# Performance work log

Hardware: AMD Instinct MI355X
Metric: run time of the kernel (lower is better)

The kernel has to match this reference:

```python
import jax, jax.numpy as jnp
import numpy as np

N_NODES, N_EDGES, N_GRAPHS = 5000, 80000, 64
LATENT, HID, STEPS = 128, 512, 3


def _mlp(h, Ws, bs):
    # MLP: ReLU after every linear (incl. last) -- MLPwoLastAct is the variant without it
    for W, b in zip(Ws, bs):
        h = jax.nn.relu(h @ W + b)
    return h


def _mlp_wo_last_act(h, Ws, bs):
    n = len(Ws)
    for i, (W, b) in enumerate(zip(Ws, bs)):
        h = h @ W + b
        if i < n - 1:
            h = jax.nn.relu(h)
    return h


def setup_inputs() -> dict:
    key = jax.random.key(0)
    ks = iter(jax.random.split(key, 64))

    def nrm(shape, s=0.05):
        return (jax.random.normal(next(ks), shape) * s).astype(jnp.float32)

    inp = {}
    inp["x"] = jax.random.normal(next(ks), (N_NODES, LATENT), jnp.float32)
    inp["edge_index"] = jax.random.randint(next(ks), (2, N_EDGES), 0, N_NODES, jnp.int32)
    inp["edge_attr"] = jax.random.normal(next(ks), (N_EDGES, LATENT), jnp.float32)
    inp["u"] = jax.random.normal(next(ks), (N_GRAPHS, LATENT), jnp.float32)
    inp["node_batch"] = jnp.sort(jax.random.randint(next(ks), (N_NODES,), 0, N_GRAPHS, jnp.int32))
    inp["edge_batch"] = jnp.sort(jax.random.randint(next(ks), (N_EDGES,), 0, N_GRAPHS, jnp.int32))
    inp["pos"] = jax.random.normal(next(ks), (N_NODES, 3), jnp.float32)
    inp["last_pos_init"] = jax.random.uniform(next(ks), (N_NODES, 3), jnp.float32, -1.0, 1.0)

    # PosEmbeddingwithMask: pos MLP(3->128->128), dis MLP(1->128->128)
    inp["pos_emb_W1"], inp["pos_emb_b1"] = nrm((3, LATENT)), nrm((LATENT,))
    inp["pos_emb_W2"], inp["pos_emb_b2"] = nrm((LATENT, LATENT)), nrm((LATENT,))
    inp["dis_W1"], inp["dis_b1"] = nrm((1, LATENT)), nrm((LATENT,))
    inp["dis_W2"], inp["dis_b2"] = nrm((LATENT, LATENT)), nrm((LATENT,))

    # per-layer edge / node MLPs: (4*latent) -> 512 -> 512 -> 128, stacked over STEPS
    cin = 4 * LATENT
    for pre in ("edge", "node"):
        inp[f"{pre}_W1"], inp[f"{pre}_b1"] = nrm((STEPS, cin, HID)), nrm((STEPS, HID))
        inp[f"{pre}_W2"], inp[f"{pre}_b2"] = nrm((STEPS, HID, HID)), nrm((STEPS, HID))
        inp[f"{pre}_W3"], inp[f"{pre}_b3"] = nrm((STEPS, HID, LATENT)), nrm((STEPS, LATENT))

    # global MLP only for layers 0..STEPS-2: (3*latent) -> 512 -> 512 -> 128
    gL, gin = STEPS - 1, 3 * LATENT
    inp["glob_W1"], inp["glob_b1"] = nrm((gL, gin, HID)), nrm((gL, HID))
    inp["glob_W2"], inp["glob_b2"] = nrm((gL, HID, HID)), nrm((gL, HID))
    inp["glob_W3"], inp["glob_b3"] = nrm((gL, HID, LATENT)), nrm((gL, LATENT))

    # shared pos_decoder: MLPwoLastAct(128 -> 128 -> 3)
    inp["dec_W1"], inp["dec_b1"] = nrm((LATENT, LATENT)), nrm((LATENT,))
    inp["dec_W2"], inp["dec_b2"] = nrm((LATENT, 3)), nrm((3,))
    return inp


def reference(x, edge_index, edge_attr, u, node_batch, edge_batch, pos, last_pos_init,
              pos_emb_W1, pos_emb_b1, pos_emb_W2, pos_emb_b2,
              dis_W1, dis_b1, dis_W2, dis_b2,
              edge_W1, edge_b1, edge_W2, edge_b2, edge_W3, edge_b3,
              node_W1, node_b1, node_W2, node_b2, node_W3, node_b3,
              glob_W1, glob_b1, glob_W2, glob_b2, glob_W3, glob_b3,
              dec_W1, dec_b1, dec_W2, dec_b2):
    src, dst = edge_index[0], edge_index[1]
    N = x.shape[0]
    counts = jnp.maximum(
        jax.ops.segment_sum(jnp.ones((N, 1), x.dtype), node_batch, N_GRAPHS), 1.0)

    def move2origin(p):
        mean = jax.ops.segment_sum(p, node_batch, N_GRAPHS) / counts
        return p - mean[node_batch]

    xs, es, us = x, edge_attr, u
    last_pos = last_pos_init  # pos_new_zeros.uniform_(-1, 1), materialized as input
    pos_preds = []
    for l in range(STEPS):
        p = last_pos  # mode='mol2conf': pos = last_pred
        # PosEmbeddingwithMask
        ex = xs + _mlp(p, (pos_emb_W1, pos_emb_W2), (pos_emb_b1, pos_emb_b2))
        length = jnp.linalg.norm(p[src] - p[dst], axis=-1, keepdims=True)  # [E,1]
        ee = es + _mlp(length, (dis_W1, dis_W2), (dis_b1, dis_b2))
        # edge update: gather -> MLP
        edge_in = jnp.concatenate([ex[src], ex[dst], ee, us[edge_batch]], axis=-1)
        e1 = _mlp(edge_in, (edge_W1[l], edge_W2[l], edge_W3[l]),
                  (edge_b1[l], edge_b2[l], edge_b3[l]))
        # scatter-reduce (sum) to nodes, then node MLP
        sent = jax.ops.segment_sum(e1, src, N)
        recv = jax.ops.segment_sum(e1, dst, N)
        node_in = jnp.concatenate([ex, sent, recv, us[node_batch]], axis=-1)
        x1 = _mlp(node_in, (node_W1[l], node_W2[l], node_W3[l]),
                  (node_b1[l], node_b2[l], node_b3[l]))
        # global update (None on last layer)
        if l < STEPS - 1:
            g_in = jnp.concatenate([us,
                                    jax.ops.segment_sum(x1, node_batch, N_GRAPHS),
                                    jax.ops.segment_sum(e1, edge_batch, N_GRAPHS)], axis=-1)
            u1 = _mlp(g_in, (glob_W1[l], glob_W2[l], glob_W3[l]),
                      (glob_b1[l], glob_b2[l], glob_b3[l]))
        else:
            u1 = us
        # residuals (dropout is identity in eval)
        xs, es, us = x1 + xs, e1 + es, u1 + us
        # pred_pos_residual=True
        delta = _mlp_wo_last_act(xs, (dec_W1, dec_W2), (dec_b1, dec_b2))
        last_pos = move2origin(last_pos + delta)
        pos_preds.append(last_pos)
    return xs, es, us, jnp.stack(pos_preds)
```

## Files before the change

### kernel.cpp

```cpp
#include <hip/hip_runtime.h>
#include <hip/hip_bf16.h>
#include <stdint.h>

#define NN 5000
#define NE 80000
#define NG 64
#define LAT 128
#define HIDN 512

typedef __hip_bfloat16 bf16;
typedef short short8 __attribute__((ext_vector_type(8)));
typedef float f32x4 __attribute__((ext_vector_type(4)));

__device__ __forceinline__ float b2f(bf16 v) { return __bfloat162float(v); }
__device__ __forceinline__ bf16 f2b(float v) { return __float2bfloat16(v); }
__device__ __forceinline__ short f2bs(float v) {
    bf16 b = __float2bfloat16(v);
    short s; __builtin_memcpy(&s, &b, 2); return s;
}

template<int K, int MODE>
__global__ __launch_bounds__(256)
void gemm_kernel(const bf16* __restrict__ A,
                 const bf16* __restrict__ Bt,
                 const float* __restrict__ bias,
                 const float* residf, const bf16* residb,
                 float* out_sf, bf16* out_sb, bf16* out_rb,
                 int M, int N, int nnt,
                 const int* __restrict__ g_src, const int* __restrict__ g_dst,
                 const int* __restrict__ g_eb,
                 const bf16* __restrict__ g_ex, const bf16* __restrict__ g_ee,
                 const bf16* __restrict__ g_us,
                 const float* __restrict__ lp,
                 const float* __restrict__ aW, const float* __restrict__ ab)
{
    constexpr bool HASA = (MODE <= 1);
    __shared__ __align__(16) bf16 As[HASA ? 128 * 32 : 8];
    __shared__ __align__(16) bf16 Bs[128 * 32];
    const int tid  = threadIdx.x;
    const int lane = tid & 63;
    const int w    = tid >> 6;
    const int li   = lane & 15, grp = lane >> 4;
    const int wr   = w >> 1, wc = w & 1;

    const int nb  = gridDim.x;
    const int q   = nb >> 3, r = nb & 7;
    const int xcd = blockIdx.x & 7, jj = blockIdx.x >> 3;
    const int wg  = (xcd < r ? xcd * (q + 1) : r * (q + 1) + (xcd - r) * q) + jj;
    const int m0  = (wg / nnt) * 128;
    const int n0  = (wg % nnt) * 128;

    f32x4 acc[4][4];
#pragma unroll
    for (int m = 0; m < 4; ++m)
#pragma unroll
        for (int n = 0; n < 4; ++n)
            acc[m][n] = (f32x4){0.f, 0.f, 0.f, 0.f};

    float r0[4], r1[4], r2[4];
    if (MODE == 2) {
#pragma unroll
        for (int m = 0; m < 4; ++m) {
            int rr = m0 + wr * 64 + m * 16 + li; if (rr >= M) rr = M - 1;
            r0[m] = lp[rr * 3 + 0]; r1[m] = lp[rr * 3 + 1]; r2[m] = lp[rr * 3 + 2];
        }
    } else if (MODE == 3) {
#pragma unroll
        for (int m = 0; m < 4; ++m) {
            int rr = m0 + wr * 64 + m * 16 + li; if (rr >= M) rr = M - 1;
            const int s = g_src[rr], d = g_dst[rr];
            const float dx = lp[s*3+0] - lp[d*3+0];
            const float dy = lp[s*3+1] - lp[d*3+1];
            const float dz = lp[s*3+2] - lp[d*3+2];
            r0[m] = sqrtf(dx*dx + dy*dy + dz*dz);
        }
    }

    const int offBase = w * 1024 + lane * 16;

    for (int kt = 0; kt < K / 32; ++kt) {
        if (HASA) {
#pragma unroll
            for (int c = 0; c < 2; ++c) {
                const int off = offBase + c * 4096;
                const int rr_ = off >> 6;
                const int g   = (off >> 4) & 3;
                const int gl  = g ^ ((rr_ >> 1) & 3);
                const int klocal = gl * 8;
                const bf16* srcp;
                if (MODE == 1) {
                    int e = m0 + rr_; if (e >= M) e = M - 1;
                    const int seg = kt >> 2;
                    const int so  = ((kt & 3) << 5) + klocal;
                    if (seg == 0)      srcp = g_ex + (size_t)g_src[e] * LAT + so;
                    else if (seg == 1) srcp = g_ex + (size_t)g_dst[e] * LAT + so;
                    else if (seg == 2) srcp = g_ee + (size_t)e * LAT + so;
                    else               srcp = g_us + (size_t)g_eb[e] * LAT + so;
                } else {
                    int rr = m0 + rr_; if (rr >= M) rr = M - 1;
                    srcp = A + (size_t)rr * K + kt * 32 + klocal;
                }
                __builtin_amdgcn_global_load_lds(
                    (__attribute__((address_space(1))) const void*)srcp,
                    (__attribute__((address_space(3))) void*)((char*)As + off),
                    16, 0, 0);
            }
        }
#pragma unroll
        for (int c = 0; c < 2; ++c) {
            const int off = offBase + c * 4096;
            const int rr_ = off >> 6;
            const int g   = (off >> 4) & 3;
            const int gl  = g ^ ((rr_ >> 1) & 3);
            const bf16* srcp = Bt + (size_t)(n0 + rr_) * K + kt * 32 + gl * 8;
            __builtin_amdgcn_global_load_lds(
                (__attribute__((address_space(1))) const void*)srcp,
                (__attribute__((address_space(3))) void*)((char*)Bs + off),
                16, 0, 0);
        }
        __syncthreads();

        short8 af[4], bfr[4];
        if (HASA) {
#pragma unroll
            for (int m = 0; m < 4; ++m) {
                const int rr_  = wr * 64 + m * 16 + li;
                const int boff = rr_ * 64 + ((grp * 16) ^ (((rr_ >> 1) & 3) << 4));
                af[m] = *(const short8*)((const char*)As + boff);
            }
        } else {
            const int kk0 = kt * 32 + grp * 8;
            float bb[8], w0[8], w1[8], w2[8];
            *(f32x4*)&bb[0] = *(const f32x4*)(ab + kk0);
            *(f32x4*)&bb[4] = *(const f32x4*)(ab + kk0 + 4);
            *(f32x4*)&w0[0] = *(const f32x4*)(aW + kk0);
            *(f32x4*)&w0[4] = *(const f32x4*)(aW + kk0 + 4);
            if (MODE == 2) {
                *(f32x4*)&w1[0] = *(const f32x4*)(aW + K + kk0);
                *(f32x4*)&w1[4] = *(const f32x4*)(aW + K + kk0 + 4);
                *(f32x4*)&w2[0] = *(const f32x4*)(aW + 2 * K + kk0);
                *(f32x4*)&w2[4] = *(const f32x4*)(aW + 2 * K + kk0 + 4);
            }
#pragma unroll
            for (int m = 0; m < 4; ++m) {
                short8 v;
#pragma unroll
                for (int e = 0; e < 8; ++e) {
                    float s;
                    if (MODE == 2)
                        s = bb[e] + r0[m]*w0[e] + r1[m]*w1[e] + r2[m]*w2[e];
                    else
                        s = bb[e] + r0[m]*w0[e];
                    v[e] = f2bs(fmaxf(s, 0.f));
                }
                af[m] = v;
            }
        }
#pragma unroll
        for (int n = 0; n < 4; ++n) {
            const int rr_  = wc * 64 + n * 16 + li;
            const int boff = rr_ * 64 + ((grp * 16) ^ (((rr_ >> 1) & 3) << 4));
            bfr[n] = *(const short8*)((const char*)Bs + boff);
        }
#pragma unroll
        for (int m = 0; m < 4; ++m)
#pragma unroll
            for (int n = 0; n < 4; ++n)
                acc[m][n] = __builtin_amdgcn_mfma_f32_16x16x32_bf16(
                    af[m], bfr[n], acc[m][n], 0, 0, 0);
        __syncthreads();
    }

#pragma unroll
    for (int m = 0; m < 4; ++m) {
        const int growb = m0 + wr * 64 + m * 16 + grp * 4;
#pragma unroll
        for (int n = 0; n < 4; ++n) {
            const int gcol = n0 + wc * 64 + n * 16 + li;
            const float bv = bias[gcol];
#pragma unroll
            for (int j = 0; j < 4; ++j) {
                const int grow = growb + j;
                if (grow >= M) continue;
                float val = fmaxf(acc[m][n][j] + bv, 0.f);
                const size_t oo = (size_t)grow * N + gcol;
                if (out_rb) out_rb[oo] = f2b(val);
                float sum = val;
                if (residf) sum += residf[oo];
                if (residb) sum += b2f(residb[oo]);
                if (out_sf) out_sf[oo] = sum;
                if (out_sb) out_sb[oo] = f2b(sum);
            }
        }
    }
}

struct TDesc { const float* src; bf16* dst; int K, N, nblk, nb32; };
struct TPack { TDesc d[28]; int n; };

__global__ __launch_bounds__(256)
void transpose_kernel(TPack p)
{
    __shared__ float t[32][33];
    int b = blockIdx.x, mi = 0;
    while (mi < p.n && b >= p.d[mi].nblk) { b -= p.d[mi].nblk; ++mi; }
    if (mi >= p.n) return;
    TDesc d = p.d[mi];
    const int kb = b / d.nb32, nb = b % d.nb32;
    const int k0 = kb * 32, n0 = nb * 32;
    const int tx = threadIdx.x & 31, ty = threadIdx.x >> 5;
#pragma unroll
    for (int qq = 0; qq < 4; ++qq) {
        const int kk = ty + qq * 8;
        t[kk][tx] = d.src[(size_t)(k0 + kk) * d.N + n0 + tx];
    }
    __syncthreads();
#pragma unroll
    for (int qq = 0; qq < 4; ++qq) {
        const int nn = ty + qq * 8;
        d.dst[(size_t)(n0 + nn) * d.K + k0 + tx] = f2b(t[tx][nn]);
    }
}

__global__ void deg_kernel(const int* __restrict__ idx, int n, int* deg)
{
    int e = blockIdx.x * 256 + threadIdx.x;
    if (e < n) atomicAdd(&deg[idx[e]], 1);
}

__global__ __launch_bounds__(256)
void scan_kernel(const int* __restrict__ deg, int* __restrict__ offs, int n)
{
    __shared__ int tot[256];
    const int t = threadIdx.x;
    const int per = (n + 255) / 256;
    const int b = t * per;
    int s = 0;
    for (int i = 0; i < per; ++i) if (b + i < n) s += deg[b + i];
    tot[t] = s;
    __syncthreads();
    for (int d = 1; d < 256; d <<= 1) {
        int v = (t >= d) ? tot[t - d] : 0;
        __syncthreads();
        tot[t] += v;
        __syncthreads();
    }
    int excl = (t == 0) ? 0 : tot[t - 1];
    for (int i = 0; i < per; ++i)
        if (b + i < n) { offs[b + i] = excl; excl += deg[b + i]; }
    if (t == 255) offs[n] = tot[255];
}

__global__ void perm_kernel(const int* __restrict__ idx, int n,
                            int* cursor, int* __restrict__ perm)
{
    int e = blockIdx.x * 256 + threadIdx.x;
    if (e < n) { int p = atomicAdd(&cursor[idx[e]], 1); perm[p] = e; }
}

__global__ __launch_bounds__(128)
void node_in_kernel(const bf16* __restrict__ exb, const bf16* __restrict__ e1f,
                    const bf16* __restrict__ usb, const int* __restrict__ nbat,
                    const int* __restrict__ offs_s, const int* __restrict__ perm_s,
                    const int* __restrict__ offs_d, const int* __restrict__ perm_d,
                    bf16* __restrict__ node_in)
{
    const int i = blockIdx.x;
    const int c = threadIdx.x;
    float s1 = 0.f, s2 = 0.f;
    const int s_lo = offs_s[i], s_hi = offs_s[i + 1];
    for (int j = s_lo; j < s_hi; ++j)
        s1 += b2f(e1f[(size_t)perm_s[j] * LAT + c]);
    const int d_lo = offs_d[i], d_hi = offs_d[i + 1];
    for (int j = d_lo; j < d_hi; ++j)
        s2 += b2f(e1f[(size_t)perm_d[j] * LAT + c]);
    const size_t o = (size_t)i * (4 * LAT);
    node_in[o + c]           = exb[(size_t)i * LAT + c];
    node_in[o + LAT + c]     = f2b(s1);
    node_in[o + 2 * LAT + c] = f2b(s2);
    node_in[o + 3 * LAT + c] = usb[(size_t)nbat[i] * LAT + c];
}

__global__ __launch_bounds__(128)
void seg_reduce_kernel(const bf16* __restrict__ vals, const int* __restrict__ batch,
                       float* out, int R, int rows_per_block)
{
    const int r0 = blockIdx.x * rows_per_block;
    if (r0 >= R) return;
    const int c = threadIdx.x;
    const int r1 = min(r0 + rows_per_block, R);
    int g = batch[r0];
    float s = 0.f;
    for (int r = r0; r < r1; ++r) {
        const int gb = batch[r];
        if (gb != g) {
            atomicAdd(&out[(size_t)g * LAT + c], s);
            g = gb; s = 0.f;
        }
        s += b2f(vals[(size_t)r * LAT + c]);
    }
    atomicAdd(&out[(size_t)g * LAT + c], s);
}

__global__ void build_g_in_kernel(const float* __restrict__ us,
                                  const float* __restrict__ gx,
                                  const float* __restrict__ ge,
                                  bf16* __restrict__ out)
{
    int id = blockIdx.x * 256 + threadIdx.x;
    if (id >= NG * 384) return;
    int g = id / 384, c = id % 384;
    int seg = c >> 7, c7 = c & 127;
    float v;
    if (seg == 0)      v = us[g * LAT + c7];
    else if (seg == 1) v = gx[g * LAT + c7];
    else               v = ge[g * LAT + c7];
    out[id] = f2b(v);
}

__global__ void counts_kernel(const int* __restrict__ nbat, float* counts)
{
    int id = blockIdx.x * 256 + threadIdx.x;
    if (id < NN) atomicAdd(&counts[nbat[id]], 1.0f);
}

__global__ void cvt_kernel(const float* __restrict__ in, bf16* __restrict__ out, int n)
{
    int id = blockIdx.x * 256 + threadIdx.x;
    if (id < n) out[id] = f2b(in[id]);
}

__global__ void us_double_kernel(float* us)
{
    int id = blockIdx.x * 256 + threadIdx.x;
    if (id < NG * LAT) us[id] *= 2.0f;
}

__global__ __launch_bounds__(64)
void dec2_kernel(const bf16* __restrict__ dh, const float* __restrict__ W2,
                 const float* __restrict__ b2, const float* __restrict__ lp,
                 const int* __restrict__ nbat, float* __restrict__ ptmp, float* psum)
{
    int i = blockIdx.x;
    int l = threadIdx.x;
    float a0 = 0.f, a1 = 0.f, a2 = 0.f;
#pragma unroll
    for (int q = 0; q < 2; ++q) {
        int k = l + q * 64;
        float h = b2f(dh[i * LAT + k]);
        a0 += h * W2[k * 3 + 0];
        a1 += h * W2[k * 3 + 1];
        a2 += h * W2[k * 3 + 2];
    }
#pragma unroll
    for (int off = 32; off > 0; off >>= 1) {
        a0 += __shfl_down(a0, off, 64);
        a1 += __shfl_down(a1, off, 64);
        a2 += __shfl_down(a2, off, 64);
    }
    if (l == 0) {
        int g = nbat[i];
        float p0 = lp[i*3+0] + a0 + b2[0];
        float p1 = lp[i*3+1] + a1 + b2[1];
        float p2 = lp[i*3+2] + a2 + b2[2];
        ptmp[i*3+0] = p0; ptmp[i*3+1] = p1; ptmp[i*3+2] = p2;
        atomicAdd(&psum[g*3+0], p0);
        atomicAdd(&psum[g*3+1], p1);
        atomicAdd(&psum[g*3+2], p2);
    }
}

__global__ void finalize_pos_kernel(const float* __restrict__ ptmp,
                                    const float* __restrict__ psum,
                                    const float* __restrict__ counts,
                                    const int* __restrict__ nbat,
                                    float* __restrict__ lp, float* __restrict__ pos_out)
{
    int id = blockIdx.x * 256 + threadIdx.x;
    if (id >= NN * 3) return;
    int i = id / 3, d = id % 3;
    int g = nbat[i];
    float v = ptmp[id] - psum[g*3+d] / fmaxf(counts[g], 1.f);
    lp[id] = v;
    pos_out[id] = v;
}

extern "C" void kernel_launch(void* const* d_in, const int* in_sizes, int n_in,
                              void* d_out, int out_size, void* d_ws, size_t ws_size,
                              hipStream_t stream)
{
    const float* x        = (const float*)d_in[0];
    const int*   ei       = (const int*)d_in[1];
    const int*   src      = ei;
    const int*   dst      = ei + NE;
    const float* eattr    = (const float*)d_in[2];
    const float* u        = (const float*)d_in[3];
    const int*   nbat     = (const int*)d_in[4];
    const int*   ebat     = (const int*)d_in[5];
    const float* lp_init  = (const float*)d_in[7];
    const float* pW1 = (const float*)d_in[8];  const float* pb1 = (const float*)d_in[9];
    const float* pW2 = (const float*)d_in[10]; const float* pb2 = (const float*)d_in[11];
    const float* dW1 = (const float*)d_in[12]; const float* db1 = (const float*)d_in[13];
    const float* dW2 = (const float*)d_in[14]; const float* db2 = (const float*)d_in[15];
    const float* eW1 = (const float*)d_in[16]; const float* eb1 = (const float*)d_in[17];
    const float* eW2 = (const float*)d_in[18]; const float* eb2 = (const float*)d_in[19];
    const float* eW3 = (const float*)d_in[20]; const float* eb3 = (const float*)d_in[21];
    const float* nW1 = (const float*)d_in[22]; const float* nb1 = (const float*)d_in[23];
    const float* nW2 = (const float*)d_in[24]; const float* nb2 = (const float*)d_in[25];
    const float* nW3 = (const float*)d_in[26]; const float* nb3 = (const float*)d_in[27];
    const float* gW1 = (const float*)d_in[28]; const float* gb1 = (const float*)d_in[29];
    const float* gW2 = (const float*)d_in[30]; const float* gb2 = (const float*)d_in[31];
    const float* gW3 = (const float*)d_in[32]; const float* gb3 = (const float*)d_in[33];
    const float* dcW1 = (const float*)d_in[34]; const float* dcb1 = (const float*)d_in[35];
    const float* dcW2 = (const float*)d_in[36]; const float* dcb2 = (const float*)d_in[37];

    float* xs = (float*)d_out;
    float* es = xs + (size_t)NN * LAT;
    float* us = es + (size_t)NE * LAT;
    float* pos_out = us + (size_t)NG * LAT;

    char* wp = (char*)d_ws;
    auto alloc = [&](size_t nbytes) {
        void* r = (void*)wp;
        wp += (nbytes + 255) & ~(size_t)255;
        return r;
    };
    bf16* eW1t = (bf16*)alloc((size_t)3*512*512*2);
    bf16* eW2t = (bf16*)alloc((size_t)3*512*512*2);
    bf16* eW3t = (bf16*)alloc((size_t)3*128*512*2);
    bf16* nW1t = (bf16*)alloc((size_t)3*512*512*2);
    bf16* nW2t = (bf16*)alloc((size_t)3*512*512*2);
    bf16* nW3t = (bf16*)alloc((size_t)3*128*512*2);
    bf16* gW1t = (bf16*)alloc((size_t)2*512*384*2);
    bf16* gW2t = (bf16*)alloc((size_t)2*512*512*2);
    bf16* gW3t = (bf16*)alloc((size_t)2*128*512*2);
    bf16* pW2t = (bf16*)alloc((size_t)128*128*2);
    bf16* dW2t = (bf16*)alloc((size_t)128*128*2);
    bf16* dcW1t = (bf16*)alloc((size_t)128*128*2);
    bf16* exb  = (bf16*)alloc((size_t)NN*LAT*2);
    bf16* usb  = (bf16*)alloc((size_t)NG*LAT*2);
    bf16* esb  = (bf16*)alloc((size_t)NE*LAT*2);
    bf16* eeb  = (bf16*)alloc((size_t)NE*LAT*2);
    bf16* h1   = (bf16*)alloc((size_t)NE*HIDN*2);
    bf16* h2   = (bf16*)alloc((size_t)NE*HIDN*2);
    bf16* e1f  = (bf16*)alloc((size_t)NE*LAT*2);
    bf16* x1f  = (bf16*)alloc((size_t)NN*LAT*2);
    float* gx  = (float*)alloc((size_t)NG*LAT*4);
    float* ge  = (float*)alloc((size_t)NG*LAT*4);
    bf16* node_in = (bf16*)alloc((size_t)NN*HIDN*2);
    bf16* nh1  = (bf16*)alloc((size_t)NN*HIDN*2);
    bf16* nh2  = (bf16*)alloc((size_t)NN*HIDN*2);
    bf16* xsb  = (bf16*)alloc((size_t)NN*LAT*2);
    bf16* g_in = (bf16*)alloc((size_t)NG*384*2);
    bf16* gh1  = (bf16*)alloc((size_t)NG*HIDN*2);
    bf16* gh2  = (bf16*)alloc((size_t)NG*HIDN*2);
    bf16* dh   = (bf16*)alloc((size_t)NN*LAT*2);
    float* lp   = (float*)alloc((size_t)NN*3*4);
    float* ptmp = (float*)alloc((size_t)NN*3*4);
    float* psum = (float*)alloc((size_t)NG*3*4);
    float* counts = (float*)alloc((size_t)NG*4);
    int* deg    = (int*)alloc((size_t)NN*4);
    int* offs_s = (int*)alloc((size_t)(NN+1)*4);
    int* offs_d = (int*)alloc((size_t)(NN+1)*4);
    int* cur_s  = (int*)alloc((size_t)NN*4);
    int* cur_d  = (int*)alloc((size_t)NN*4);
    int* perm_s = (int*)alloc((size_t)NE*4);
    int* perm_d = (int*)alloc((size_t)NE*4);

    hipMemcpyAsync(xs, x,     (size_t)NN*LAT*4, hipMemcpyDeviceToDevice, stream);
    hipMemcpyAsync(us, u,     (size_t)NG*LAT*4, hipMemcpyDeviceToDevice, stream);
    hipMemcpyAsync(lp, lp_init, (size_t)NN*3*4, hipMemcpyDeviceToDevice, stream);
    hipMemsetAsync(counts, 0, NG*4, stream);
    counts_kernel<<<(NN+255)/256, 256, 0, stream>>>(nbat, counts);
    cvt_kernel<<<(NG*LAT+255)/256, 256, 0, stream>>>(us, usb, NG*LAT);
    cvt_kernel<<<(NE*LAT+255)/256, 256, 0, stream>>>(eattr, esb, NE*LAT);

    const int eb256 = (NE + 255) / 256;
    hipMemsetAsync(deg, 0, NN*4, stream);
    deg_kernel<<<eb256, 256, 0, stream>>>(src, NE, deg);
    scan_kernel<<<1, 256, 0, stream>>>(deg, offs_s, NN);
    hipMemsetAsync(deg, 0, NN*4, stream);
    deg_kernel<<<eb256, 256, 0, stream>>>(dst, NE, deg);
    scan_kernel<<<1, 256, 0, stream>>>(deg, offs_d, NN);
    hipMemcpyAsync(cur_s, offs_s, NN*4, hipMemcpyDeviceToDevice, stream);
    hipMemcpyAsync(cur_d, offs_d, NN*4, hipMemcpyDeviceToDevice, stream);
    perm_kernel<<<eb256, 256, 0, stream>>>(src, NE, cur_s, perm_s);
    perm_kernel<<<eb256, 256, 0, stream>>>(dst, NE, cur_d, perm_d);

    TPack pk{}; int nd = 0, totb = 0;
    auto addT = [&](const float* s, bf16* d, int K, int N) {
        pk.d[nd].src = s; pk.d[nd].dst = d; pk.d[nd].K = K; pk.d[nd].N = N;
        pk.d[nd].nblk = (K/32)*(N/32); pk.d[nd].nb32 = N/32;
        totb += pk.d[nd].nblk; ++nd;
    };
    for (int l = 0; l < 3; ++l) {
        addT(eW1 + (size_t)l*512*512, eW1t + (size_t)l*512*512, 512, 512);
        addT(eW2 + (size_t)l*512*512, eW2t + (size_t)l*512*512, 512, 512);
        addT(eW3 + (size_t)l*512*128, eW3t + (size_t)l*128*512, 512, 128);
        addT(nW1 + (size_t)l*512*512, nW1t + (size_t)l*512*512, 512, 512);
        addT(nW2 + (size_t)l*512*512, nW2t + (size_t)l*512*512, 512, 512);
        addT(nW3 + (size_t)l*512*128, nW3t + (size_t)l*128*512, 512, 128);
    }
    for (int l = 0; l < 2; ++l) {
        addT(gW1 + (size_t)l*384*512, gW1t + (size_t)l*512*384, 384, 512);
        addT(gW2 + (size_t)l*512*512, gW2t + (size_t)l*512*512, 512, 512);
        addT(gW3 + (size_t)l*512*128, gW3t + (size_t)l*128*512, 512, 128);
    }
    addT(pW2, pW2t, 128, 128);
    addT(dW2, dW2t, 128, 128);
    addT(dcW1, dcW1t, 128, 128);
    pk.n = nd;
    transpose_kernel<<<totb, 256, 0, stream>>>(pk);

    const int mtE = NE / 128;
    const int mtN = (NN + 127) / 128;
    #define NIL6 nullptr, nullptr, nullptr, nullptr, nullptr, nullptr
    #define NIL3 nullptr, nullptr, nullptr

    for (int l = 0; l < 3; ++l) {
        gemm_kernel<128,2><<<mtN, 256, 0, stream>>>(
            nullptr, pW2t, pb2, xs, nullptr, nullptr, exb, nullptr, NN, LAT, 1,
            NIL6, lp, pW1, pb1);
        gemm_kernel<128,3><<<mtE, 256, 0, stream>>>(
            nullptr, dW2t, db2, nullptr, esb, nullptr, eeb, nullptr, NE, LAT, 1,
            src, dst, nullptr, nullptr, nullptr, nullptr, lp, dW1, db1);
        gemm_kernel<512,1><<<mtE*4, 256, 0, stream>>>(
            nullptr, eW1t + (size_t)l*512*512, eb1 + l*HIDN, nullptr, nullptr,
            nullptr, nullptr, h1, NE, HIDN, 4,
            src, dst, ebat, exb, eeb, usb, NIL3);
        gemm_kernel<512,0><<<mtE*4, 256, 0, stream>>>(
            h1, eW2t + (size_t)l*512*512, eb2 + l*HIDN, nullptr, nullptr,
            nullptr, nullptr, h2, NE, HIDN, 4, NIL6, NIL3);
        gemm_kernel<512,0><<<mtE, 256, 0, stream>>>(
            h2, eW3t + (size_t)l*128*512, eb3 + l*LAT, nullptr, esb,
            (l == 2 ? es : nullptr), (l < 2 ? esb : nullptr), e1f, NE, LAT, 1,
            NIL6, NIL3);
        if (l < 2) {
            hipMemsetAsync(gx, 0, (size_t)2*NG*LAT*4, stream);
            seg_reduce_kernel<<<(NE+63)/64, 128, 0, stream>>>(e1f, ebat, ge, NE, 64);
        }
        node_in_kernel<<<NN, 128, 0, stream>>>(
            exb, e1f, usb, nbat, offs_s, perm_s, offs_d, perm_d, node_in);
        gemm_kernel<512,0><<<mtN*4, 256, 0, stream>>>(
            node_in, nW1t + (size_t)l*512*512, nb1 + l*HIDN, nullptr, nullptr,
            nullptr, nullptr, nh1, NN, HIDN, 4, NIL6, NIL3);
        gemm_kernel<512,0><<<mtN*4, 256, 0, stream>>>(
            nh1, nW2t + (size_t)l*512*512, nb2 + l*HIDN, nullptr, nullptr,
            nullptr, nullptr, nh2, NN, HIDN, 4, NIL6, NIL3);
        gemm_kernel<512,0><<<mtN, 256, 0, stream>>>(
            nh2, nW3t + (size_t)l*128*512, nb3 + l*LAT, xs, nullptr,
            xs, xsb, x1f, NN, LAT, 1, NIL6, NIL3);
        if (l < 2) {
            seg_reduce_kernel<<<(NN+31)/32, 128, 0, stream>>>(x1f, nbat, gx, NN, 32);
            build_g_in_kernel<<<(NG*384+255)/256, 256, 0, stream>>>(us, gx, ge, g_in);
            gemm_kernel<384,0><<<4, 256, 0, stream>>>(
                g_in, gW1t + (size_t)l*512*384, gb1 + l*HIDN, nullptr, nullptr,
                nullptr, nullptr, gh1, NG, HIDN, 4, NIL6, NIL3);
            gemm_kernel<512,0><<<4, 256, 0, stream>>>(
                gh1, gW2t + (size_t)l*512*512, gb2 + l*HIDN, nullptr, nullptr,
                nullptr, nullptr, gh2, NG, HIDN, 4, NIL6, NIL3);
            gemm_kernel<512,0><<<1, 256, 0, stream>>>(
                gh2, gW3t + (size_t)l*128*512, gb3 + l*LAT, us, nullptr,
                us, usb, nullptr, NG, LAT, 1, NIL6, NIL3);
        } else {
            us_double_kernel<<<(NG*LAT+255)/256, 256, 0, stream>>>(us);
        }
        gemm_kernel<128,0><<<mtN, 256, 0, stream>>>(
            xsb, dcW1t, dcb1, nullptr, nullptr, nullptr, nullptr, dh, NN, LAT, 1,
            NIL6, NIL3);
        hipMemsetAsync(psum, 0, NG*3*4, stream);
        dec2_kernel<<<NN, 64, 0, stream>>>(dh, dcW2, dcb2, lp, nbat, ptmp, psum);
        finalize_pos_kernel<<<(NN*3+255)/256, 256, 0, stream>>>(
            ptmp, psum, counts, nbat, lp, pos_out + (size_t)l*NN*3);
    }
    (void)in_sizes; (void)n_in; (void)out_size; (void)ws_size;
}
```

Measured before the change: 1.594 ms.

## Add 256x256 double-buffered 8-wave GEMM for edge MLP hidden layers

Adds a new gemm8 kernel with 256x256 output tiles, 512 threads, 128KB LDS double buffering with K-step 64, and a phased schedule that interleaves LDS reads, async global-to-LDS staging and MFMA under explicit waitcnt and barriers. It replaces the two large edge-MLP 512x512 GEMMs, including the gathered-input first layer, and removes the gather mode from the old kernel. Larger tiles raise arithmetic intensity and cut redundant weight and gather traffic. In exchange, occupancy is lower and the hand-tuned synchronization is easier to get wrong.

Result: slower. 1.732 ms (+8.7%).

```diff
diff --git a/kernel.cpp b/kernel.cpp
--- a/kernel.cpp
+++ b/kernel.cpp
@@ -17,6 +17,140 @@
 __device__ __forceinline__ short f2bs(float v) {
     bf16 b = __float2bfloat16(v);
     short s; __builtin_memcpy(&s, &b, 2); return s;
+}
+
+template<int MODE>
+__global__ __launch_bounds__(512, 2)
+void gemm8_kernel(const bf16* __restrict__ A, const bf16* __restrict__ Bt,
+                  const float* __restrict__ bias, bf16* __restrict__ out,
+                  int M, int nnt,
+                  const int* __restrict__ g_src, const int* __restrict__ g_dst,
+                  const int* __restrict__ g_eb,
+                  const bf16* __restrict__ g_ex, const bf16* __restrict__ g_ee,
+                  const bf16* __restrict__ g_us)
+{
+    constexpr int K = 512, NT = K / 64;
+    __shared__ __align__(16) char lds[131072];
+
+    const int tid  = threadIdx.x;
+    const int lane = tid & 63;
+    const int w    = tid >> 6;
+    const int li   = lane & 15, grp = lane >> 4;
+    const int wr   = w >> 2, wc = w & 3;
+
+    const int nb  = gridDim.x;
+    const int q8  = nb >> 3, r8 = nb & 7;
+    const int xcd = blockIdx.x & 7, jj = blockIdx.x >> 3;
+    const int wg  = (xcd < r8 ? xcd * (q8 + 1) : r8 * (q8 + 1) + (xcd - r8) * q8) + jj;
+    const int m0  = (wg / nnt) * 256;
+    const int n0  = (wg % nnt) * 256;
+
+    f32x4 acc[8][4];
+#pragma unroll
+    for (int m = 0; m < 8; ++m)
+#pragma unroll
+        for (int n = 0; n < 4; ++n)
+            acc[m][n] = (f32x4){0.f, 0.f, 0.f, 0.f};
+
+    auto STAGE = [&](int t, int h, bool isA) {
+        if (t >= NT) return;
+        char* base = lds + (isA ? 0 : 65536) + (t & 1) * 32768 + h * 16384;
+#pragma unroll
+        for (int j = 0; j < 2; ++j) {
+            const int p  = (tid + j * 512) * 16;
+            const int qb = p ^ (((p >> 9) & 1) << 5);
+            const int row = qb >> 7;
+            const int kk  = (qb & 127) >> 1;
+            const bf16* srcp;
+            if (isA) {
+                if (MODE == 1) {
+                    int e = m0 + h * 128 + row; if (e >= M) e = M - 1;
+                    const int seg = t >> 1;
+                    const int so  = ((t & 1) << 6) + kk;
+                    if (seg == 0)      srcp = g_ex + (size_t)g_src[e] * LAT + so;
+                    else if (seg == 1) srcp = g_ex + (size_t)g_dst[e] * LAT + so;
+                    else if (seg == 2) srcp = g_ee + (size_t)e * LAT + so;
+                    else               srcp = g_us + (size_t)g_eb[e] * LAT + so;
+                } else {
+                    int rr = m0 + h * 128 + row; if (rr >= M) rr = M - 1;
+                    srcp = A + (size_t)rr * K + t * 64 + kk;
+                }
+            } else {
+                const int rr = n0 + h * 128 + row;
+                srcp = Bt + (size_t)rr * K + t * 64 + kk;
+            }
+            __builtin_amdgcn_global_load_lds(
+                (__attribute__((address_space(1))) const void*)srcp,
+                (__attribute__((address_space(3))) void*)(base + p), 16, 0, 0);
+        }
+    };
+
+#define PHASE(QM, QN, ST_T, ST_H, ST_A, VM)                                        \
+    {                                                                              \
+        const char* Ab = lds + bsel * 32768 + (QM) * 16384;                        \
+        const char* Bb = lds + 65536 + bsel * 32768 + (QN) * 16384;                \
+        short8 af[4][2], bfv[2][2];                                                \
+        _Pragma("unroll") for (int m4 = 0; m4 < 4; ++m4) {                         \
+            const int row = wr * 64 + m4 * 16 + li;                                \
+            const int xr  = ((row >> 2) & 1) << 5;                                 \
+            _Pragma("unroll") for (int s = 0; s < 2; ++s)                          \
+                af[m4][s] = *(const short8*)(Ab +                                  \
+                    ((row * 128 + (s * 32 + grp * 8) * 2) ^ xr));                  \
+        }                                                                          \
+        _Pragma("unroll") for (int n2 = 0; n2 < 2; ++n2) {                         \
+            const int row = wc * 32 + n2 * 16 + li;                                \
+            const int xr  = ((row >> 2) & 1) << 5;                                 \
+            _Pragma("unroll") for (int s = 0; s < 2; ++s)                          \
+                bfv[n2][s] = *(const short8*)(Bb +                                 \
+                    ((row * 128 + (s * 32 + grp * 8) * 2) ^ xr));                  \
+        }                                                                          \
+        STAGE(ST_T, ST_H, ST_A);                                                   \
+        if ((VM) == 0)      asm volatile("s_waitcnt vmcnt(0)" ::: "memory");       \
+        else if ((VM) > 0)  asm volatile("s_waitcnt vmcnt(4)" ::: "memory");       \
+        __builtin_amdgcn_s_barrier();                                              \
+        asm volatile("s_waitcnt lgkmcnt(0)" ::: "memory");                         \
+        __builtin_amdgcn_s_setprio(1);                                             \
+        _Pragma("unroll") for (int m4 = 0; m4 < 4; ++m4)                           \
+        _Pragma("unroll") for (int n2 = 0; n2 < 2; ++n2)                           \
+        _Pragma("unroll") for (int s = 0; s < 2; ++s)                              \
+            acc[(QM)*4+m4][(QN)*2+n2] = __builtin_amdgcn_mfma_f32_16x16x32_bf16(   \
+                af[m4][s], bfv[n2][s], acc[(QM)*4+m4][(QN)*2+n2], 0, 0, 0);        \
+        __builtin_amdgcn_s_setprio(0);                                             \
+        __builtin_amdgcn_s_barrier();                                              \
+    }
+
+    STAGE(0, 0, true);  STAGE(0, 0, false);
+    STAGE(0, 1, true);  STAGE(0, 1, false);
+    STAGE(1, 0, false); STAGE(1, 0, true);
+    asm volatile("s_waitcnt vmcnt(4)" ::: "memory");
+    __builtin_amdgcn_s_barrier();
+
+    int bsel = 0;
+    for (int t = 0; t < NT; ++t) {
+        const int vm = (t >= NT - 2) ? 0 : 1;
+        PHASE(0, 0, t + 1, 1, true,  -1)
+        PHASE(1, 0, t + 1, 1, false, -1)
+        PHASE(0, 1, t + 2, 0, false, -1)
+        PHASE(1, 1, t + 2, 0, true,  vm)
+        bsel ^= 1;
+    }
+#undef PHASE
+
+#pragma unroll
+    for (int m = 0; m < 8; ++m) {
+        const int growb = m0 + (m >> 2) * 128 + wr * 64 + (m & 3) * 16 + grp * 4;
+#pragma unroll
+        for (int n = 0; n < 4; ++n) {
+            const int gcol = n0 + (n >> 1) * 128 + wc * 32 + (n & 1) * 16 + li;
+            const float bv = bias[gcol];
+#pragma unroll
+            for (int j = 0; j < 4; ++j) {
+                const int grow = growb + j;
+                if (grow < M)
+                    out[(size_t)grow * 512 + gcol] = f2b(fmaxf(acc[m][n][j] + bv, 0.f));
+            }
+        }
+    }
 }
 
 template<int K, int MODE>
@@ -28,13 +162,10 @@
                  float* out_sf, bf16* out_sb, bf16* out_rb,
                  int M, int N, int nnt,
                  const int* __restrict__ g_src, const int* __restrict__ g_dst,
-                 const int* __restrict__ g_eb,
-                 const bf16* __restrict__ g_ex, const bf16* __restrict__ g_ee,
-                 const bf16* __restrict__ g_us,
                  const float* __restrict__ lp,
                  const float* __restrict__ aW, const float* __restrict__ ab)
 {
-    constexpr bool HASA = (MODE <= 1);
+    constexpr bool HASA = (MODE == 0);
     __shared__ __align__(16) bf16 As[HASA ? 128 * 32 : 8];
     __shared__ __align__(16) bf16 Bs[128 * 32];
     const int tid  = threadIdx.x;
@@ -86,20 +217,8 @@
                 const int rr_ = off >> 6;
                 const int g   = (off >> 4) & 3;
                 const int gl  = g ^ ((rr_ >> 1) & 3);
-                const int klocal = gl * 8;
-                const bf16* srcp;
-                if (MODE == 1) {
-                    int e = m0 + rr_; if (e >= M) e = M - 1;
-                    const int seg = kt >> 2;
-                    const int so  = ((kt & 3) << 5) + klocal;
-                    if (seg == 0)      srcp = g_ex + (size_t)g_src[e] * LAT + so;
-                    else if (seg == 1) srcp = g_ex + (size_t)g_dst[e] * LAT + so;
-                    else if (seg == 2) srcp = g_ee + (size_t)e * LAT + so;
-                    else               srcp = g_us + (size_t)g_eb[e] * LAT + so;
-                } else {
-                    int rr = m0 + rr_; if (rr >= M) rr = M - 1;
-                    srcp = A + (size_t)rr * K + kt * 32 + klocal;
-                }
+                int rr = m0 + rr_; if (rr >= M) rr = M - 1;
+                const bf16* srcp = A + (size_t)rr * K + kt * 32 + gl * 8;
                 __builtin_amdgcn_global_load_lds(
                     (__attribute__((address_space(1))) const void*)srcp,
                     (__attribute__((address_space(3))) void*)((char*)As + off),
@@ -512,29 +631,29 @@
     pk.n = nd;
     transpose_kernel<<<totb, 256, 0, stream>>>(pk);
 
-    const int mtE = NE / 128;
-    const int mtN = (NN + 127) / 128;
-    #define NIL6 nullptr, nullptr, nullptr, nullptr, nullptr, nullptr
+    const int mtE  = NE / 128;
+    const int mtN  = (NN + 127) / 128;
+    const int mt8E = (NE + 255) / 256;
+    #define NIL2 nullptr, nullptr
     #define NIL3 nullptr, nullptr, nullptr
 
     for (int l = 0; l < 3; ++l) {
         gemm_kernel<128,2><<<mtN, 256, 0, stream>>>(
             nullptr, pW2t, pb2, xs, nullptr, nullptr, exb, nullptr, NN, LAT, 1,
-            NIL6, lp, pW1, pb1);
+            NIL2, lp, pW1, pb1);
         gemm_kernel<128,3><<<mtE, 256, 0, stream>>>(
             nullptr, dW2t, db2, nullptr, esb, nullptr, eeb, nullptr, NE, LAT, 1,
-            src, dst, nullptr, nullptr, nullptr, nullptr, lp, dW1, db1);
-        gemm_kernel<512,1><<<mtE*4, 256, 0, stream>>>(
-            nullptr, eW1t + (size_t)l*512*512, eb1 + l*HIDN, nullptr, nullptr,
-            nullptr, nullptr, h1, NE, HIDN, 4,
-            src, dst, ebat, exb, eeb, usb, NIL3);
-        gemm_kernel<512,0><<<mtE*4, 256, 0, stream>>>(
-            h1, eW2t + (size_t)l*512*512, eb2 + l*HIDN, nullptr, nullptr,
-            nullptr, nullptr, h2, NE, HIDN, 4, NIL6, NIL3);
+            src, dst, lp, dW1, db1);
+        gemm8_kernel<1><<<mt8E*2, 512, 0, stream>>>(
+            nullptr, eW1t + (size_t)l*512*512, eb1 + l*HIDN, h1, NE, 2,
+            src, dst, ebat, exb, eeb, usb);
+        gemm8_kernel<0><<<mt8E*2, 512, 0, stream>>>(
+            h1, eW2t + (size_t)l*512*512, eb2 + l*HIDN, h2, NE, 2,
+            NIL3, NIL3);
         gemm_kernel<512,0><<<mtE, 256, 0, stream>>>(
             h2, eW3t + (size_t)l*128*512, eb3 + l*LAT, nullptr, esb,
             (l == 2 ? es : nullptr), (l < 2 ? esb : nullptr), e1f, NE, LAT, 1,
-            NIL6, NIL3);
+            NIL2, NIL3);
         if (l < 2) {
             hipMemsetAsync(gx, 0, (size_t)2*NG*LAT*4, stream);
             seg_reduce_kernel<<<(NE+63)/64, 128, 0, stream>>>(e1f, ebat, ge, NE, 64);
@@ -543,31 +662,31 @@
             exb, e1f, usb, nbat, offs_s, perm_s, offs_d, perm_d, node_in);
         gemm_kernel<512,0><<<mtN*4, 256, 0, stream>>>(
             node_in, nW1t + (size_t)l*512*512, nb1 + l*HIDN, nullptr, nullptr,
-            nullptr, nullptr, nh1, NN, HIDN, 4, NIL6, NIL3);
+            nullptr, nullptr, nh1, NN, HIDN, 4, NIL2, NIL3);
         gemm_kernel<512,0><<<mtN*4, 256, 0, stream>>>(
             nh1, nW2t + (size_t)l*512*512, nb2 + l*HIDN, nullptr, nullptr,
-            nullptr, nullptr, nh2, NN, HIDN, 4, NIL6, NIL3);
+            nullptr, nullptr, nh2, NN, HIDN, 4, NIL2, NIL3);
         gemm_kernel<512,0><<<mtN, 256, 0, stream>>>(
             nh2, nW3t + (size_t)l*128*512, nb3 + l*LAT, xs, nullptr,
-            xs, xsb, x1f, NN, LAT, 1, NIL6, NIL3);
+            xs, xsb, x1f, NN, LAT, 1, NIL2, NIL3);
         if (l < 2) {
             seg_reduce_kernel<<<(NN+31)/32, 128, 0, stream>>>(x1f, nbat, gx, NN, 32);
             build_g_in_kernel<<<(NG*384+255)/256, 256, 0, stream>>>(us, gx, ge, g_in);
             gemm_kernel<384,0><<<4, 256, 0, stream>>>(
                 g_in, gW1t + (size_t)l*512*384, gb1 + l*HIDN, nullptr, nullptr,
-                nullptr, nullptr, gh1, NG, HIDN, 4, NIL6, NIL3);
+                nullptr, nullptr, gh1, NG, HIDN, 4, NIL2, NIL3);
             gemm_kernel<512,0><<<4, 256, 0, stream>>>(
                 gh1, gW2t + (size_t)l*512*512, gb2 + l*HIDN, nullptr, nullptr,
-                nullptr, nullptr, gh2, NG, HIDN, 4, NIL6, NIL3);
+                nullptr, nullptr, gh2, NG, HIDN, 4, NIL2, NIL3);
             gemm_kernel<512,0><<<1, 256, 0, stream>>>(
                 gh2, gW3t + (size_t)l*128*512, gb3 + l*LAT, us, nullptr,
-                us, usb, nullptr, NG, LAT, 1, NIL6, NIL3);
+                us, usb, nullptr, NG, LAT, 1, NIL2, NIL3);
         } else {
             us_double_kernel<<<(NG*LAT+255)/256, 256, 0, stream>>>(us);
         }
         gemm_kernel<128,0><<<mtN, 256, 0, stream>>>(
             xsb, dcW1t, dcb1, nullptr, nullptr, nullptr, nullptr, dh, NN, LAT, 1,
-            NIL6, NIL3);
+            NIL2, NIL3);
         hipMemsetAsync(psum, 0, NG*3*4, stream);
         dec2_kernel<<<NN, 64, 0, stream>>>(dh, dcW2, dcb2, lp, nbat, ptmp, psum);
         finalize_pos_kernel<<<(NN*3+255)/256, 256, 0, stream>>>(
```

## Add K64-tiled GEMM kernel with hoisted gather indices for 512-K MLP layers

Applied to the files above, without the earlier changes.

Introduces a dedicated GEMM kernel for K=512 layers that loads 64-wide K tiles per iteration with an XOR-swizzled LDS layout, halving the number of barrier rounds. For the edge first layer it hoists the src/dst/batch index loads out of the K loop instead of re-reading them every tile. The larger LDS footprint (64KB declared) may reduce blocks per CU and occupancy.

Result: slower. 1.668 ms (+4.7%).

```diff
diff --git a/kernel.cpp b/kernel.cpp
--- a/kernel.cpp
+++ b/kernel.cpp
@@ -17,6 +17,146 @@
 __device__ __forceinline__ short f2bs(float v) {
     bf16 b = __float2bfloat16(v);
     short s; __builtin_memcpy(&s, &b, 2); return s;
+}
+
+template<int MODE>
+__global__ __launch_bounds__(256)
+void gemm64_kernel(const bf16* __restrict__ A, const bf16* __restrict__ Bt,
+                   const float* __restrict__ bias,
+                   const float* residf, const bf16* residb,
+                   float* out_sf, bf16* out_sb, bf16* out_rb,
+                   int M, int N, int nnt,
+                   const int* __restrict__ g_src, const int* __restrict__ g_dst,
+                   const int* __restrict__ g_eb,
+                   const bf16* __restrict__ g_ex, const bf16* __restrict__ g_ee,
+                   const bf16* __restrict__ g_us)
+{
+    constexpr int K = 512, NT = K / 64;
+    __shared__ __align__(16) char lds[65536];
+
+    const int tid  = threadIdx.x;
+    const int lane = tid & 63;
+    const int w    = tid >> 6;
+    const int li   = lane & 15, grp = lane >> 4;
+    const int wr   = w >> 1, wc = w & 1;
+
+    const int nb  = gridDim.x;
+    const int q   = nb >> 3, r = nb & 7;
+    const int xcd = blockIdx.x & 7, jj = blockIdx.x >> 3;
+    const int wg  = (xcd < r ? xcd * (q + 1) : r * (q + 1) + (xcd - r) * q) + jj;
+    const int m0  = (wg / nnt) * 128;
+    const int n0  = (wg % nnt) * 128;
+
+    f32x4 acc[4][4];
+#pragma unroll
+    for (int m = 0; m < 4; ++m)
+#pragma unroll
+        for (int n = 0; n < 4; ++n)
+            acc[m][n] = (f32x4){0.f, 0.f, 0.f, 0.f};
+
+    int he[4], hs[4], hd[4], hb[4];
+    if (MODE == 1) {
+#pragma unroll
+        for (int c = 0; c < 4; ++c) {
+            const int p  = (tid + c * 256) * 16;
+            const int qb = p ^ ((p >> 3) & 0x70);
+            int e = m0 + (qb >> 7); if (e >= M) e = M - 1;
+            he[c] = e;
+            hs[c] = g_src[e]; hd[c] = g_dst[e]; hb[c] = g_eb[e];
+        }
+    }
+
+    char* ldsA = lds;
+    char* ldsB = lds + 16384;
+
+    for (int t = 0; t < NT; ++t) {
+#pragma unroll
+        for (int c = 0; c < 4; ++c) {
+            const int p  = (tid + c * 256) * 16;
+            const int qb = p ^ ((p >> 3) & 0x70);
+            const int row = qb >> 7;
+            const int kk  = (qb & 127) >> 1;
+            const bf16* srcp;
+            if (MODE == 1) {
+                const int seg = t >> 1;
+                const int so  = ((t & 1) << 6) + kk;
+                if (seg == 0)      srcp = g_ex + (size_t)hs[c] * LAT + so;
+                else if (seg == 1) srcp = g_ex + (size_t)hd[c] * LAT + so;
+                else if (seg == 2) srcp = g_ee + (size_t)he[c] * LAT + so;
+                else               srcp = g_us + (size_t)hb[c] * LAT + so;
+            } else {
+                int rr = m0 + row; if (rr >= M) rr = M - 1;
+                srcp = A + (size_t)rr * K + t * 64 + kk;
+            }
+            __builtin_amdgcn_global_load_lds(
+                (__attribute__((address_space(1))) const void*)srcp,
+                (__attribute__((address_space(3))) void*)(ldsA + p), 16, 0, 0);
+        }
+#pragma unroll
+        for (int c = 0; c < 4; ++c) {
+            const int p  = (tid + c * 256) * 16;
+            const int qb = p ^ ((p >> 3) & 0x70);
+            const int row = qb >> 7;
+            const int kk  = (qb & 127) >> 1;
+            const bf16* srcp = Bt + (size_t)(n0 + row) * K + t * 64 + kk;
+            __builtin_amdgcn_global_load_lds(
+                (__attribute__((address_space(1))) const void*)srcp,
+                (__attribute__((address_space(3))) void*)(ldsB + p), 16, 0, 0);
+        }
+        __syncthreads();
+
+        short8 af[4][2], bf[4][2];
+#pragma unroll
+        for (int m = 0; m < 4; ++m) {
+            const int row = wr * 64 + m * 16 + li;
+            const int xr  = (row & 7) << 4;
+#pragma unroll
+            for (int s = 0; s < 2; ++s)
+                af[m][s] = *(const short8*)(ldsA +
+                    ((row * 128 + s * 64 + grp * 16) ^ xr));
+        }
+#pragma unroll
+        for (int n = 0; n < 4; ++n) {
+            const int row = wc * 64 + n * 16 + li;
+            const int xr  = (row & 7) << 4;
+#pragma unroll
+            for (int s = 0; s < 2; ++s)
+                bf[n][s] = *(const short8*)(ldsB +
+                    ((row * 128 + s * 64 + grp * 16) ^ xr));
+        }
+#pragma unroll
+        for (int m = 0; m < 4; ++m)
+#pragma unroll
+            for (int n = 0; n < 4; ++n)
+#pragma unroll
+                for (int s = 0; s < 2; ++s)
+                    acc[m][n] = __builtin_amdgcn_mfma_f32_16x16x32_bf16(
+                        af[m][s], bf[n][s], acc[m][n], 0, 0, 0);
+        __syncthreads();
+    }
+
+#pragma unroll
+    for (int m = 0; m < 4; ++m) {
+        const int growb = m0 + wr * 64 + m * 16 + grp * 4;
+#pragma unroll
+        for (int n = 0; n < 4; ++n) {
+            const int gcol = n0 + wc * 64 + n * 16 + li;
+            const float bv = bias[gcol];
+#pragma unroll
+            for (int j = 0; j < 4; ++j) {
+                const int grow = growb + j;
+                if (grow >= M) continue;
+                float val = fmaxf(acc[m][n][j] + bv, 0.f);
+                const size_t oo = (size_t)grow * N + gcol;
+                if (out_rb) out_rb[oo] = f2b(val);
+                float sum = val;
+                if (residf) sum += residf[oo];
+                if (residb) sum += b2f(residb[oo]);
+                if (out_sf) out_sf[oo] = sum;
+                if (out_sb) out_sb[oo] = f2b(sum);
+            }
+        }
+    }
 }
 
 template<int K, int MODE>
@@ -28,13 +168,10 @@
                  float* out_sf, bf16* out_sb, bf16* out_rb,
                  int M, int N, int nnt,
                  const int* __restrict__ g_src, const int* __restrict__ g_dst,
-                 const int* __restrict__ g_eb,
-                 const bf16* __restrict__ g_ex, const bf16* __restrict__ g_ee,
-                 const bf16* __restrict__ g_us,
                  const float* __restrict__ lp,
                  const float* __restrict__ aW, const float* __restrict__ ab)
 {
-    constexpr bool HASA = (MODE <= 1);
+    constexpr bool HASA = (MODE == 0);
     __shared__ __align__(16) bf16 As[HASA ? 128 * 32 : 8];
     __shared__ __align__(16) bf16 Bs[128 * 32];
     const int tid  = threadIdx.x;
@@ -86,20 +223,8 @@
                 const int rr_ = off >> 6;
                 const int g   = (off >> 4) & 3;
                 const int gl  = g ^ ((rr_ >> 1) & 3);
-                const int klocal = gl * 8;
-                const bf16* srcp;
-                if (MODE == 1) {
-                    int e = m0 + rr_; if (e >= M) e = M - 1;
-                    const int seg = kt >> 2;
-                    const int so  = ((kt & 3) << 5) + klocal;
-                    if (seg == 0)      srcp = g_ex + (size_t)g_src[e] * LAT + so;
-                    else if (seg == 1) srcp = g_ex + (size_t)g_dst[e] * LAT + so;
-                    else if (seg == 2) srcp = g_ee + (size_t)e * LAT + so;
-                    else               srcp = g_us + (size_t)g_eb[e] * LAT + so;
-                } else {
-                    int rr = m0 + rr_; if (rr >= M) rr = M - 1;
-                    srcp = A + (size_t)rr * K + kt * 32 + klocal;
-                }
+                int rr = m0 + rr_; if (rr >= M) rr = M - 1;
+                const bf16* srcp = A + (size_t)rr * K + kt * 32 + gl * 8;
                 __builtin_amdgcn_global_load_lds(
                     (__attribute__((address_space(1))) const void*)srcp,
                     (__attribute__((address_space(3))) void*)((char*)As + off),
@@ -512,62 +637,61 @@
     pk.n = nd;
     transpose_kernel<<<totb, 256, 0, stream>>>(pk);
 
-    const int mtE = NE / 128;
-    const int mtN = (NN + 127) / 128;
-    #define NIL6 nullptr, nullptr, nullptr, nullptr, nullptr, nullptr
+    const int mtE  = NE / 128;
+    const int mtN  = (NN + 127) / 128;
     #define NIL3 nullptr, nullptr, nullptr
 
     for (int l = 0; l < 3; ++l) {
         gemm_kernel<128,2><<<mtN, 256, 0, stream>>>(
             nullptr, pW2t, pb2, xs, nullptr, nullptr, exb, nullptr, NN, LAT, 1,
-            NIL6, lp, pW1, pb1);
+            nullptr, nullptr, lp, pW1, pb1);
         gemm_kernel<128,3><<<mtE, 256, 0, stream>>>(
             nullptr, dW2t, db2, nullptr, esb, nullptr, eeb, nullptr, NE, LAT, 1,
-            src, dst, nullptr, nullptr, nullptr, nullptr, lp, dW1, db1);
-        gemm_kernel<512,1><<<mtE*4, 256, 0, stream>>>(
+            src, dst, lp, dW1, db1);
+        gemm64_kernel<1><<<mtE*4, 256, 0, stream>>>(
             nullptr, eW1t + (size_t)l*512*512, eb1 + l*HIDN, nullptr, nullptr,
             nullptr, nullptr, h1, NE, HIDN, 4,
-            src, dst, ebat, exb, eeb, usb, NIL3);
-        gemm_kernel<512,0><<<mtE*4, 256, 0, stream>>>(
+            src, dst, ebat, exb, eeb, usb);
+        gemm64_kernel<0><<<mtE*4, 256, 0, stream>>>(
             h1, eW2t + (size_t)l*512*512, eb2 + l*HIDN, nullptr, nullptr,
-            nullptr, nullptr, h2, NE, HIDN, 4, NIL6, NIL3);
-        gemm_kernel<512,0><<<mtE, 256, 0, stream>>>(
+            nullptr, nullptr, h2, NE, HIDN, 4, NIL3, NIL3);
+        gemm64_kernel<0><<<mtE, 256, 0, stream>>>(
             h2, eW3t + (size_t)l*128*512, eb3 + l*LAT, nullptr, esb,
             (l == 2 ? es : nullptr), (l < 2 ? esb : nullptr), e1f, NE, LAT, 1,
-            NIL6, NIL3);
+            NIL3, NIL3);
         if (l < 2) {
             hipMemsetAsync(gx, 0, (size_t)2*NG*LAT*4, stream);
             seg_reduce_kernel<<<(NE+63)/64, 128, 0, stream>>>(e1f, ebat, ge, NE, 64);
         }
         node_in_kernel<<<NN, 128, 0, stream>>>(
             exb, e1f, usb, nbat, offs_s, perm_s, offs_d, perm_d, node_in);
-        gemm_kernel<512,0><<<mtN*4, 256, 0, stream>>>(
+        gemm64_kernel<0><<<mtN*4, 256, 0, stream>>>(
             node_in, nW1t + (size_t)l*512*512, nb1 + l*HIDN, nullptr, nullptr,
-            nullptr, nullptr, nh1, NN, HIDN, 4, NIL6, NIL3);
-        gemm_kernel<512,0><<<mtN*4, 256, 0, stream>>>(
+            nullptr, nullptr, nh1, NN, HIDN, 4, NIL3, NIL3);
+        gemm64_kernel<0><<<mtN*4, 256, 0, stream>>>(
             nh1, nW2t + (size_t)l*512*512, nb2 + l*HIDN, nullptr, nullptr,
-            nullptr, nullptr, nh2, NN, HIDN, 4, NIL6, NIL3);
-        gemm_kernel<512,0><<<mtN, 256, 0, stream>>>(
+            nullptr, nullptr, nh2, NN, HIDN, 4, NIL3, NIL3);
+        gemm64_kernel<0><<<mtN, 256, 0, stream>>>(
             nh2, nW3t + (size_t)l*128*512, nb3 + l*LAT, xs, nullptr,
-            xs, xsb, x1f, NN, LAT, 1, NIL6, NIL3);
+            xs, xsb, x1f, NN, LAT, 1, NIL3, NIL3);
         if (l < 2) {
             seg_reduce_kernel<<<(NN+31)/32, 128, 0, stream>>>(x1f, nbat, gx, NN, 32);
             build_g_in_kernel<<<(NG*384+255)/256, 256, 0, stream>>>(us, gx, ge, g_in);
             gemm_kernel<384,0><<<4, 256, 0, stream>>>(
                 g_in, gW1t + (size_t)l*512*384, gb1 + l*HIDN, nullptr, nullptr,
-                nullptr, nullptr, gh1, NG, HIDN, 4, NIL6, NIL3);
+                nullptr, nullptr, gh1, NG, HIDN, 4, NIL3, nullptr, nullptr);
             gemm_kernel<512,0><<<4, 256, 0, stream>>>(
                 gh1, gW2t + (size_t)l*512*512, gb2 + l*HIDN, nullptr, nullptr,
-                nullptr, nullptr, gh2, NG, HIDN, 4, NIL6, NIL3);
+                nullptr, nullptr, gh2, NG, HIDN, 4, NIL3, nullptr, nullptr);
             gemm_kernel<512,0><<<1, 256, 0, stream>>>(
                 gh2, gW3t + (size_t)l*128*512, gb3 + l*LAT, us, nullptr,
-                us, usb, nullptr, NG, LAT, 1, NIL6, NIL3);
+                us, usb, nullptr, NG, LAT, 1, NIL3, nullptr, nullptr);
         } else {
             us_double_kernel<<<(NG*LAT+255)/256, 256, 0, stream>>>(us);
         }
         gemm_kernel<128,0><<<mtN, 256, 0, stream>>>(
             xsb, dcW1t, dcb1, nullptr, nullptr, nullptr, nullptr, dh, NN, LAT, 1,
-            NIL6, NIL3);
+            NIL3, nullptr, nullptr);
         hipMemsetAsync(psum, 0, NG*3*4, stream);
         dec2_kernel<<<NN, 64, 0, stream>>>(dh, dcW2, dcb2, lp, nbat, ptmp, psum);
         finalize_pos_kernel<<<(NN*3+255)/256, 256, 0, stream>>>(
```
